# Optimization experiments

Measured on AMD Instinct MI355X. Metric: run time of the kernel, lower is better.

The kernel has to match this reference:

```python
import jax, jax.numpy as jnp
import numpy as np

D_MODEL = 1024
NUM_HEADS = 16
HEAD_DIM = D_MODEL // NUM_HEADS
ROPE_THETA = 10000.0


def apply_rope(x, positions):
    # x: (B, H, S, Dh), positions: (S,) int
    half = x.shape[-1] // 2
    inv_freq = ROPE_THETA ** (-jnp.arange(half, dtype=jnp.float32) * 2.0 / x.shape[-1])  # (Dh/2,)
    ang = positions.astype(jnp.float32)[:, None] * inv_freq[None, :]  # (S, Dh/2)
    cos, sin = jnp.cos(ang), jnp.sin(ang)
    x1 = x[..., 0::2]  # (B,H,S,Dh/2)
    x2 = x[..., 1::2]
    r1 = x1 * cos - x2 * sin
    r2 = x1 * sin + x2 * cos
    return jnp.stack([r1, r2], axis=-1).reshape(x.shape)


def setup_inputs() -> dict:
    key = jax.random.key(0)
    ks = jax.random.split(key, 5)
    B, S = 2, 2048
    scale = 1.0 / np.sqrt(D_MODEL)
    x = jax.random.normal(ks[0], (B, S, D_MODEL), dtype=jnp.float32)
    Wq = jax.random.normal(ks[1], (D_MODEL, D_MODEL), dtype=jnp.float32) * scale
    Wk = jax.random.normal(ks[2], (D_MODEL, D_MODEL), dtype=jnp.float32) * scale
    Wv = jax.random.normal(ks[3], (D_MODEL, D_MODEL), dtype=jnp.float32) * scale
    Wo = jax.random.normal(ks[4], (D_MODEL, D_MODEL), dtype=jnp.float32) * scale
    token_positions = jnp.arange(S, dtype=jnp.int32)
    return {"x": x, "token_positions": token_positions, "Wq": Wq, "Wk": Wk, "Wv": Wv, "Wo": Wo}


def reference(x, token_positions, Wq, Wk, Wv, Wo):
    B, S, _ = x.shape
    # Linear is bias-free: y = x @ W.T (W: [out, in])
    def proj(W):
        y = jnp.einsum('bsd,ed->bse', x, W)
        return y.reshape(B, S, NUM_HEADS, HEAD_DIM).transpose(0, 2, 1, 3)  # (B,H,S,Dh)
    q, k, v = proj(Wq), proj(Wk), proj(Wv)
    q = apply_rope(q, token_positions)
    k = apply_rope(k, token_positions)
    scores = jnp.einsum('bhqd,bhkd->bhqk', q, k) / jnp.sqrt(jnp.float32(HEAD_DIM))
    causal = jnp.tril(jnp.ones((S, S), dtype=bool))
    scores = jnp.where(causal, scores, -jnp.inf)
    attn = jax.nn.softmax(scores, axis=-1)
    out = jnp.einsum('bhqk,bhkd->bhqd', attn, v)  # (B,H,S,Dh)
    out = out.transpose(0, 2, 1, 3).reshape(B, S, D_MODEL)
    return jnp.einsum('bsd,ed->bse', out, Wo)
```

## Files before the change

kernel.cpp:

```cpp
#include <hip/hip_runtime.h>


typedef unsigned short u16;
typedef unsigned int   u32;
typedef unsigned long long u64;
using s16x8 = __attribute__((ext_vector_type(8))) short;
using f32x4 = __attribute__((ext_vector_type(4))) float;

__device__ __forceinline__ u16 f2bf(float f) {
  union { float f; u32 u; } v; v.f = f;
  return (u16)((v.u + 0x7fffu + ((v.u >> 16) & 1u)) >> 16);
}
__device__ __forceinline__ float bf2f(u16 h) {
  union { u32 u; float f; } v; v.u = ((u32)h) << 16;
  return v.f;
}

__device__ __forceinline__ void gl2lds(const u16* g, u16* l) {
  __builtin_amdgcn_global_load_lds(
      (const __attribute__((address_space(1))) void*)g,
      (__attribute__((address_space(3))) void*)l, 16, 0, 0);
}

__global__ __launch_bounds__(256) void cvt_all(
    const float* __restrict__ x,
    const float* __restrict__ wq, const float* __restrict__ wk,
    const float* __restrict__ wv, const float* __restrict__ wo,
    u16* __restrict__ xb, u16* __restrict__ wqb, u16* __restrict__ wkb,
    u16* __restrict__ wvb, u16* __restrict__ wob,
    float* __restrict__ rtab, const int* __restrict__ pos) {
  int bid = blockIdx.x;
  if (bid >= 8192) {
    int idx = (bid - 8192) * 256 + threadIdx.x;
    int s = idx >> 5, pair = idx & 31;
    float p = (float)pos[s];
    float freq = __expf(-0.28782313662425572f * (float)pair);
    float sn, cs;
    sincosf(p * freq, &sn, &cs);
    *(float2*)(rtab + idx * 2) = make_float2(cs, sn);
    return;
  }
  int e = (bid * 256 + threadIdx.x) * 4;
  const float* src; u16* dst; int off;
  const int XN = 4 << 20;
  if (e < XN) { src = x; dst = xb; off = e; }
  else {
    int t = e - XN; int sel = t >> 20; off = t & ((1 << 20) - 1);
    src = sel == 0 ? wq : sel == 1 ? wk : sel == 2 ? wv : wo;
    dst = sel == 0 ? wqb : sel == 1 ? wkb : sel == 2 ? wvb : wob;
  }
  float4 v = *(const float4*)(src + off);
  ushort4 o;
  o.x = f2bf(v.x); o.y = f2bf(v.y); o.z = f2bf(v.z); o.w = f2bf(v.w);
  *(ushort4*)(dst + off) = o;
}

__device__ __forceinline__ void gemm_core(
    const u16* __restrict__ A, const u16* __restrict__ W,
    u16* As, u16* Bs, int bm0, int bn0, int kb, int ke, f32x4 (&acc)[4][4]) {
  const int K = 1024;
  int tid = threadIdx.x;
  int wid = tid >> 6, lane = tid & 63, quad = lane >> 4, l15 = lane & 15;
  int wm = (wid >> 1) * 64, wn = (wid & 1) * 64;
  int ch0 = wid * 128 + lane, ch1 = ch0 + 64;
  int r0 = ch0 >> 2, c0 = (ch0 & 3) * 8;
  int r1 = ch1 >> 2, c1 = (ch1 & 3) * 8;
  const u16* Ab = A + (size_t)bm0 * K;
  const u16* Wb = W + (size_t)bn0 * K;
  u16* lA0 = As + wid * 1024; u16* lA1 = lA0 + 512;
  u16* lB0 = Bs + wid * 1024; u16* lB1 = lB0 + 512;
  for (int k0 = kb; k0 < ke; k0 += 32) {
    __syncthreads();
    gl2lds(Ab + (size_t)r0 * K + k0 + c0, lA0);
    gl2lds(Ab + (size_t)r1 * K + k0 + c1, lA1);
    gl2lds(Wb + (size_t)r0 * K + k0 + c0, lB0);
    gl2lds(Wb + (size_t)r1 * K + k0 + c1, lB1);
    __syncthreads();
    s16x8 af[4], bf[4];
#pragma unroll
    for (int mi = 0; mi < 4; mi++)
      af[mi] = *(const s16x8*)(As + (wm + mi * 16 + l15) * 32 + quad * 8);
#pragma unroll
    for (int ni = 0; ni < 4; ni++)
      bf[ni] = *(const s16x8*)(Bs + (wn + ni * 16 + l15) * 32 + quad * 8);
#pragma unroll
    for (int mi = 0; mi < 4; mi++)
#pragma unroll
      for (int ni = 0; ni < 4; ni++)
        acc[mi][ni] = __builtin_amdgcn_mfma_f32_16x16x32_bf16(
            af[mi], bf[ni], acc[mi][ni], 0, 0, 0);
  }
}

template <bool TAB>
__global__ __launch_bounds__(256) void gemm_qkv_t(
    const u16* __restrict__ xb,
    const u16* __restrict__ wq, const u16* __restrict__ wk,
    const u16* __restrict__ wv, const int* __restrict__ pos,
    const float* __restrict__ rtab,
    u16* __restrict__ qh, u16* __restrict__ kh, u16* __restrict__ vt) {
  __shared__ __align__(16) u16 As[128 * 32];
  __shared__ __align__(16) u16 Bs[128 * 32];
  __shared__ __align__(16) float tabl[TAB ? 2 : 128 * 32 * 2];
  int z = blockIdx.z;
  const u16* W = (z == 0) ? wq : (z == 1) ? wk : wv;
  int bm0 = blockIdx.y * 128, bn0 = blockIdx.x * 128;
  int tid = threadIdx.x;
  if (!TAB && z < 2) {
    for (int idx = tid; idx < 4096; idx += 256) {
      int rl = idx >> 5, pair = idx & 31;
      int s = (bm0 + rl) & 2047;
      float p = (float)pos[s];
      float freq = __expf(-0.28782313662425572f * (float)pair);
      float sn, cs;
      sincosf(p * freq, &sn, &cs);
      tabl[idx * 2] = cs;
      tabl[idx * 2 + 1] = sn;
    }
  }
  f32x4 acc[4][4];
  const f32x4 fz = {0.f, 0.f, 0.f, 0.f};
#pragma unroll
  for (int mi = 0; mi < 4; mi++)
#pragma unroll
    for (int ni = 0; ni < 4; ni++) acc[mi][ni] = fz;
  gemm_core(xb, W, As, Bs, bm0, bn0, 0, 1024, acc);
  int wid = tid >> 6, lane = tid & 63;
  int quad = lane >> 4, l15 = lane & 15;
  int wm = (wid >> 1) * 64, wn = (wid & 1) * 64;
  if (z < 2) {
    u16* dst = (z == 0) ? qh : kh;
    float qs = (z == 0) ? 0.125f : 1.0f;
#pragma unroll
    for (int mi = 0; mi < 4; mi++)
#pragma unroll
      for (int ni = 0; ni < 4; ni++) {
        int col = bn0 + wn + ni * 16 + l15;
        int h = col >> 6, d = col & 63;
        int pairi = d >> 1;
        int odd = d & 1;
#pragma unroll
        for (int r = 0; r < 4; r++) {
          int rl = wm + mi * 16 + quad * 4 + r;
          int row = bm0 + rl;
          int b = row >> 11, s = row & 2047;
          float v0 = acc[mi][ni][r];
          float vp = __shfl_xor(v0, 1, 64);
          float cs, sn;
          if (TAB) {
            float2 t = *(const float2*)(rtab + (size_t)(s * 32 + pairi) * 2);
            cs = t.x; sn = t.y;
          } else {
            cs = tabl[(rl * 32 + pairi) * 2];
            sn = tabl[(rl * 32 + pairi) * 2 + 1];
          }
          float o = odd ? (vp * sn + v0 * cs) : (v0 * cs - vp * sn);
          dst[(((size_t)(b * 16 + h)) * 2048 + s) * 64 + d] = f2bf(o * qs);
        }
      }
  } else {
#pragma unroll
    for (int mi = 0; mi < 4; mi++)
#pragma unroll
      for (int ni = 0; ni < 4; ni++) {
        int row0 = bm0 + wm + mi * 16 + quad * 4;
        int col = bn0 + wn + ni * 16 + l15;
        int b = row0 >> 11, s0 = row0 & 2047, h = col >> 6, d = col & 63;
        u64 pk = (u64)f2bf(acc[mi][ni][0]) |
                 ((u64)f2bf(acc[mi][ni][1]) << 16) |
                 ((u64)f2bf(acc[mi][ni][2]) << 32) |
                 ((u64)f2bf(acc[mi][ni][3]) << 48);
        *(u64*)(vt + (((size_t)(b * 16 + h)) * 64 + d) * 2048 + s0) = pk;
      }
  }
}

__global__ __launch_bounds__(256) void gemm_out_sk(
    const u16* __restrict__ ao, const u16* __restrict__ wo,
    float* __restrict__ pbuf) {
  __shared__ __align__(16) u16 As[128 * 32];
  __shared__ __align__(16) u16 Bs[128 * 32];
  int bm0 = blockIdx.y * 128, bn0 = blockIdx.x * 128;
  int kb = blockIdx.z * 512;
  f32x4 acc[4][4];
  const f32x4 fz = {0.f, 0.f, 0.f, 0.f};
#pragma unroll
  for (int mi = 0; mi < 4; mi++)
#pragma unroll
    for (int ni = 0; ni < 4; ni++) acc[mi][ni] = fz;
  gemm_core(ao, wo, As, Bs, bm0, bn0, kb, kb + 512, acc);
  int tid = threadIdx.x, wid = tid >> 6, lane = tid & 63;
  int quad = lane >> 4, l15 = lane & 15;
  int wm = (wid >> 1) * 64, wn = (wid & 1) * 64;
  float* dst = pbuf + (size_t)blockIdx.z * (4u << 20);
#pragma unroll
  for (int mi = 0; mi < 4; mi++)
#pragma unroll
    for (int ni = 0; ni < 4; ni++)
#pragma unroll
      for (int r = 0; r < 4; r++) {
        int row = bm0 + wm + mi * 16 + quad * 4 + r;
        int col = bn0 + wn + ni * 16 + l15;
        dst[(size_t)row * 1024 + col] = acc[mi][ni][r];
      }
}

__global__ __launch_bounds__(256) void add_out(
    const float* __restrict__ p, float* __restrict__ o) {
  int i = (blockIdx.x * 256 + threadIdx.x) * 4;
  float4 a = *(const float4*)(p + i);
  float4 b = *(const float4*)(p + (4u << 20) + i);
  float4 r;
  r.x = a.x + b.x; r.y = a.y + b.y; r.z = a.z + b.z; r.w = a.w + b.w;
  *(float4*)(o + i) = r;
}

__global__ __launch_bounds__(256) void gemm_out(
    const u16* __restrict__ ao, const u16* __restrict__ wo,
    float* __restrict__ out) {
  __shared__ __align__(16) u16 As[128 * 32];
  __shared__ __align__(16) u16 Bs[128 * 32];
  int bm0 = blockIdx.y * 128, bn0 = blockIdx.x * 128;
  f32x4 acc[4][4];
  const f32x4 fz = {0.f, 0.f, 0.f, 0.f};
#pragma unroll
  for (int mi = 0; mi < 4; mi++)
#pragma unroll
    for (int ni = 0; ni < 4; ni++) acc[mi][ni] = fz;
  gemm_core(ao, wo, As, Bs, bm0, bn0, 0, 1024, acc);
  int tid = threadIdx.x, wid = tid >> 6, lane = tid & 63;
  int quad = lane >> 4, l15 = lane & 15;
  int wm = (wid >> 1) * 64, wn = (wid & 1) * 64;
#pragma unroll
  for (int mi = 0; mi < 4; mi++)
#pragma unroll
    for (int ni = 0; ni < 4; ni++)
#pragma unroll
      for (int r = 0; r < 4; r++) {
        int row = bm0 + wm + mi * 16 + quad * 4 + r;
        int col = bn0 + wn + ni * 16 + l15;
        out[(size_t)row * 1024 + col] = acc[mi][ni][r];
      }
}

#define KTS 72
#define VTS 72
#define PTS 40
#define OTS 72

__global__ __launch_bounds__(256, 4) void attn_k(
    const u16* __restrict__ qh, const u16* __restrict__ kh,
    const u16* __restrict__ vt, u16* __restrict__ ao) {
  __shared__ __align__(16) u16 ks[64 * KTS];
  __shared__ __align__(16) u16 vs[64 * VTS];
  __shared__ __align__(16) u16 pt[4 * 16 * PTS];
  int bid = blockIdx.x;
  int bh = bid & 31, pi = bid >> 5;
  int b = bh >> 4, h = bh & 15;
  int tid = threadIdx.x, wid = tid >> 6, lane = tid & 63;
  int quad = lane >> 4, l15 = lane & 15;
  int qsub = wid & 1, thalf = wid >> 1;
  const u16* qbase = qh + (size_t)bh * 2048 * 64;
  const u16* kbase = kh + (size_t)bh * 2048 * 64;
  const u16* vbase = vt + (size_t)bh * 64 * 2048;
  u16* ptw = pt + wid * 16 * PTS;
  const f32x4 fz = {0.f, 0.f, 0.f, 0.f};
  int srow = tid >> 2, sc = (tid & 3) * 8;

#pragma unroll
  for (int phase = 0; phase < 2; phase++) {
    int qt = phase ? (63 - pi) : pi;
    int q0 = qt * 32, q0w = q0 + qsub * 16;
    s16x8 qf0 = *(const s16x8*)(qbase + (size_t)(q0w + l15) * 64 + quad * 8);
    s16x8 qf1 = *(const s16x8*)(qbase + (size_t)(q0w + l15) * 64 + 32 + quad * 8);
    f32x4 acc[4];
#pragma unroll
    for (int md = 0; md < 4; md++) acc[md] = fz;
    float lsum = 0.f;
    int qg = q0w + l15;
    int nt = (qt >> 1) + 1;
    uint4 rk0 = *(const uint4*)(kbase + (size_t)srow * 64 + sc);
    uint4 rk1 = *(const uint4*)(kbase + (size_t)srow * 64 + sc + 32);
    uint4 rv0 = *(const uint4*)(vbase + (size_t)srow * 2048 + sc);
    uint4 rv1 = *(const uint4*)(vbase + (size_t)srow * 2048 + sc + 32);
    for (int it = 0; it < nt; it++) {
      __syncthreads();
      *(uint4*)(ks + srow * KTS + sc) = rk0;
      *(uint4*)(ks + srow * KTS + sc + 32) = rk1;
      *(uint4*)(vs + srow * VTS + sc) = rv0;
      *(uint4*)(vs + srow * VTS + sc + 32) = rv1;
      if (it + 1 < nt) {
        int t1 = (it + 1) << 6;
        rk0 = *(const uint4*)(kbase + (size_t)(t1 + srow) * 64 + sc);
        rk1 = *(const uint4*)(kbase + (size_t)(t1 + srow) * 64 + sc + 32);
        rv0 = *(const uint4*)(vbase + (size_t)srow * 2048 + t1 + sc);
        rv1 = *(const uint4*)(vbase + (size_t)srow * 2048 + t1 + sc + 32);
      }
      __syncthreads();
      int t0 = it << 6, tb = thalf * 32;
      bool diag = (it == nt - 1);
#pragma unroll
      for (int mt = 0; mt < 2; mt++) {
        int krow = tb + mt * 16 + l15;
        s16x8 ka0 = *(const s16x8*)(ks + krow * KTS + quad * 8);
        s16x8 ka1 = *(const s16x8*)(ks + krow * KTS + 32 + quad * 8);
        f32x4 st = __builtin_amdgcn_mfma_f32_16x16x32_bf16(ka0, qf0, fz, 0, 0, 0);
        st = __builtin_amdgcn_mfma_f32_16x16x32_bf16(ka1, qf1, st, 0, 0, 0);
        u64 pk = 0;
#pragma unroll
        for (int r = 0; r < 4; r++) {
          float p = __expf(st[r]);
          if (diag) {
            int tg = t0 + tb + mt * 16 + quad * 4 + r;
            if (tg > qg) p = 0.f;
          }
          lsum += p;
          pk |= ((u64)f2bf(p)) << (16 * r);
        }
        *(u64*)(ptw + l15 * PTS + mt * 16 + quad * 4) = pk;
      }
      s16x8 pb = *(const s16x8*)(ptw + l15 * PTS + quad * 8);
#pragma unroll
      for (int md = 0; md < 4; md++) {
        s16x8 va = *(const s16x8*)(vs + (md * 16 + l15) * VTS + tb + quad * 8);
        acc[md] = __builtin_amdgcn_mfma_f32_16x16x32_bf16(va, pb, acc[md], 0, 0, 0);
      }
    }
    lsum += __shfl_xor(lsum, 16, 64);
    lsum += __shfl_xor(lsum, 32, 64);
    __syncthreads();
    float* redo = (float*)ks;
    float* redl = (float*)vs;
    if (thalf == 1) {
#pragma unroll
      for (int md = 0; md < 4; md++)
#pragma unroll
        for (int r = 0; r < 4; r++)
          redo[(qsub * 64 + lane) * 16 + md * 4 + r] = acc[md][r];
      redl[qsub * 64 + lane] = lsum;
    }
    __syncthreads();
    if (thalf == 0) {
#pragma unroll
      for (int md = 0; md < 4; md++)
#pragma unroll
        for (int r = 0; r < 4; r++)
          acc[md][r] += redo[(qsub * 64 + lane) * 16 + md * 4 + r];
      lsum += redl[qsub * 64 + lane];
      float rl = 1.0f / lsum;
      u16* ow = pt + qsub * 16 * OTS;
#pragma unroll
      for (int md = 0; md < 4; md++) {
        u64 ok = 0;
#pragma unroll
        for (int r = 0; r < 4; r++)
          ok |= ((u64)f2bf(acc[md][r] * rl)) << (16 * r);
        *(u64*)(ow + l15 * OTS + md * 16 + quad * 4) = ok;
      }
      int qq = lane >> 2, dc = lane & 3;
      uint4 o0 = *(uint4*)(ow + qq * OTS + dc * 16);
      uint4 o1 = *(uint4*)(ow + qq * OTS + dc * 16 + 8);
      size_t orow = (size_t)b * 2048 + q0 + qsub * 16 + qq;
      *(uint4*)(ao + orow * 1024 + h * 64 + dc * 16) = o0;
      *(uint4*)(ao + orow * 1024 + h * 64 + dc * 16 + 8) = o1;
    }
  }
}

extern "C" void kernel_launch(void* const* d_in, const int* in_sizes, int n_in,
                              void* d_out, int out_size, void* d_ws,
                              size_t ws_size, hipStream_t stream) {
  const float* x  = (const float*)d_in[0];
  const int* pos  = (const int*)d_in[1];
  const float* Wq = (const float*)d_in[2];
  const float* Wk = (const float*)d_in[3];
  const float* Wv = (const float*)d_in[4];
  const float* Wo = (const float*)d_in[5];
  float* out = (float*)d_out;

  char* ws = (char*)d_ws;
  const size_t MB = 1u << 20;
  u16* xb  = (u16*)(ws);
  u16* wqb = (u16*)(ws + 8 * MB);
  u16* wkb = (u16*)(ws + 10 * MB);
  u16* wvb = (u16*)(ws + 12 * MB);
  u16* wob = (u16*)(ws + 14 * MB);
  u16* qhb = (u16*)(ws + 16 * MB);
  u16* khb = (u16*)(ws + 24 * MB);
  u16* vtb = (u16*)(ws + 32 * MB);
  float* rtab = (float*)(ws + 40 * MB);
  float* pbuf = (float*)(ws + 41 * MB);
  u16* ao  = xb;

  bool tabok = ws_size >= 41 * MB;
  bool skok  = ws_size >= 73 * MB;

  cvt_all<<<tabok ? 8448 : 8192, 256, 0, stream>>>(
      x, Wq, Wk, Wv, Wo, xb, wqb, wkb, wvb, wob, rtab, pos);
  if (tabok)
    gemm_qkv_t<true><<<dim3(8, 32, 3), 256, 0, stream>>>(
        xb, wqb, wkb, wvb, pos, rtab, qhb, khb, vtb);
  else
    gemm_qkv_t<false><<<dim3(8, 32, 3), 256, 0, stream>>>(
        xb, wqb, wkb, wvb, pos, rtab, qhb, khb, vtb);
  attn_k<<<1024, 256, 0, stream>>>(qhb, khb, vtb, ao);
  if (skok) {
    gemm_out_sk<<<dim3(8, 32, 2), 256, 0, stream>>>(ao, wob, pbuf);
    add_out<<<4096, 256, 0, stream>>>(pbuf, out);
  } else {
    gemm_out<<<dim3(8, 32), 256, 0, stream>>>(ao, wob, out);
  }
}
```

Measured before the change: 207.5 us.

## Remap GEMM block order, stage QK epilogue through LDS, widen attention blocks

The QKV and output GEMMs now remap the linear block index so consecutive blocks are spread across tiles, aiming for better cache and XCD locality. The Q/K RoPE epilogue writes to a padded LDS tile first and then issues coalesced 16-byte stores, replacing scattered 2-byte global writes. The attention kernel moves to 512-thread blocks covering 64 query rows, so each K/V tile loaded into LDS is shared by twice as many queries. That halves the grid to 512 blocks and adds LDS use, which may reduce occupancy and makes the diagonal tile larger.

```diff
diff --git a/kernel.cpp b/kernel.cpp
--- a/kernel.cpp
+++ b/kernel.cpp
@@ -101,10 +101,13 @@
     u16* __restrict__ qh, u16* __restrict__ kh, u16* __restrict__ vt) {
   __shared__ __align__(16) u16 As[128 * 32];
   __shared__ __align__(16) u16 Bs[128 * 32];
+  __shared__ __align__(16) u16 ob[128 * 136];
   __shared__ __align__(16) float tabl[TAB ? 2 : 128 * 32 * 2];
-  int z = blockIdx.z;
+  int id = blockIdx.x + 8 * blockIdx.y + 256 * blockIdx.z;
+  int nid = (id & 7) * 96 + (id >> 3);
+  int bx = nid & 7, by = (nid >> 3) & 31, z = nid >> 8;
   const u16* W = (z == 0) ? wq : (z == 1) ? wk : wv;
-  int bm0 = blockIdx.y * 128, bn0 = blockIdx.x * 128;
+  int bm0 = by * 128, bn0 = bx * 128;
   int tid = threadIdx.x;
   if (!TAB && z < 2) {
     for (int idx = tid; idx < 4096; idx += 256) {
@@ -135,15 +138,13 @@
     for (int mi = 0; mi < 4; mi++)
 #pragma unroll
       for (int ni = 0; ni < 4; ni++) {
-        int col = bn0 + wn + ni * 16 + l15;
-        int h = col >> 6, d = col & 63;
-        int pairi = d >> 1;
-        int odd = d & 1;
+        int col = wn + ni * 16 + l15;
+        int d = (bn0 + col) & 63;
+        int pairi = d >> 1, odd = d & 1;
 #pragma unroll
         for (int r = 0; r < 4; r++) {
           int rl = wm + mi * 16 + quad * 4 + r;
-          int row = bm0 + rl;
-          int b = row >> 11, s = row & 2047;
+          int s = (bm0 + rl) & 2047;
           float v0 = acc[mi][ni][r];
           float vp = __shfl_xor(v0, 1, 64);
           float cs, sn;
@@ -155,9 +156,21 @@
             sn = tabl[(rl * 32 + pairi) * 2 + 1];
           }
           float o = odd ? (vp * sn + v0 * cs) : (v0 * cs - vp * sn);
-          dst[(((size_t)(b * 16 + h)) * 2048 + s) * 64 + d] = f2bf(o * qs);
+          ob[rl * 136 + col] = f2bf(o * qs);
         }
       }
+    __syncthreads();
+#pragma unroll
+    for (int k2 = 0; k2 < 8; k2++) {
+      int idx = tid + 256 * k2;
+      int row = idx >> 4, seg = idx & 15;
+      uint4 w = *(const uint4*)(ob + row * 136 + seg * 8);
+      int grow = bm0 + row;
+      int b2 = grow >> 11, s2 = grow & 2047;
+      int gc = bn0 + seg * 8;
+      int h2 = gc >> 6, d2 = gc & 63;
+      *(uint4*)(dst + (((size_t)(b2 * 16 + h2)) * 2048 + s2) * 64 + d2) = w;
+    }
   } else {
 #pragma unroll
     for (int mi = 0; mi < 4; mi++)
@@ -180,8 +193,11 @@
     float* __restrict__ pbuf) {
   __shared__ __align__(16) u16 As[128 * 32];
   __shared__ __align__(16) u16 Bs[128 * 32];
-  int bm0 = blockIdx.y * 128, bn0 = blockIdx.x * 128;
-  int kb = blockIdx.z * 512;
+  int id = blockIdx.x + 8 * blockIdx.y + 256 * blockIdx.z;
+  int nid = (id & 7) * 64 + (id >> 3);
+  int bx = nid & 7, by = (nid >> 3) & 31, z = nid >> 8;
+  int bm0 = by * 128, bn0 = bx * 128;
+  int kb = z * 512;
   f32x4 acc[4][4];
   const f32x4 fz = {0.f, 0.f, 0.f, 0.f};
 #pragma unroll
@@ -192,7 +208,7 @@
   int tid = threadIdx.x, wid = tid >> 6, lane = tid & 63;
   int quad = lane >> 4, l15 = lane & 15;
   int wm = (wid >> 1) * 64, wn = (wid & 1) * 64;
-  float* dst = pbuf + (size_t)blockIdx.z * (4u << 20);
+  float* dst = pbuf + (size_t)z * (4u << 20);
 #pragma unroll
   for (int mi = 0; mi < 4; mi++)
 #pragma unroll
@@ -248,29 +264,32 @@
 #define PTS 40
 #define OTS 72
 
-__global__ __launch_bounds__(256, 4) void attn_k(
+__global__ __launch_bounds__(512, 4) void attn_k(
     const u16* __restrict__ qh, const u16* __restrict__ kh,
     const u16* __restrict__ vt, u16* __restrict__ ao) {
-  __shared__ __align__(16) u16 ks[64 * KTS];
-  __shared__ __align__(16) u16 vs[64 * VTS];
-  __shared__ __align__(16) u16 pt[4 * 16 * PTS];
+  __shared__ __align__(16) u16 kv[64 * KTS + 64 * VTS];
+  __shared__ __align__(16) u16 pt[8 * 16 * PTS];
+  __shared__ __align__(16) float redl2[256];
+  u16* ks = kv;
+  u16* vs = kv + 64 * KTS;
   int bid = blockIdx.x;
   int bh = bid & 31, pi = bid >> 5;
   int b = bh >> 4, h = bh & 15;
   int tid = threadIdx.x, wid = tid >> 6, lane = tid & 63;
   int quad = lane >> 4, l15 = lane & 15;
-  int qsub = wid & 1, thalf = wid >> 1;
+  int qsub = wid & 3, thalf = wid >> 2;
   const u16* qbase = qh + (size_t)bh * 2048 * 64;
   const u16* kbase = kh + (size_t)bh * 2048 * 64;
   const u16* vbase = vt + (size_t)bh * 64 * 2048;
   u16* ptw = pt + wid * 16 * PTS;
   const f32x4 fz = {0.f, 0.f, 0.f, 0.f};
-  int srow = tid >> 2, sc = (tid & 3) * 8;
+  int srow = tid >> 3, sc = (tid & 7) * 8;
+  int tb = thalf * 32;
 
 #pragma unroll
   for (int phase = 0; phase < 2; phase++) {
-    int qt = phase ? (63 - pi) : pi;
-    int q0 = qt * 32, q0w = q0 + qsub * 16;
+    int qt = phase ? (31 - pi) : pi;
+    int q0 = qt * 64, q0w = q0 + qsub * 16;
     s16x8 qf0 = *(const s16x8*)(qbase + (size_t)(q0w + l15) * 64 + quad * 8);
     s16x8 qf1 = *(const s16x8*)(qbase + (size_t)(q0w + l15) * 64 + 32 + quad * 8);
     f32x4 acc[4];
@@ -278,26 +297,20 @@
     for (int md = 0; md < 4; md++) acc[md] = fz;
     float lsum = 0.f;
     int qg = q0w + l15;
-    int nt = (qt >> 1) + 1;
+    int nt = qt + 1;
     uint4 rk0 = *(const uint4*)(kbase + (size_t)srow * 64 + sc);
-    uint4 rk1 = *(const uint4*)(kbase + (size_t)srow * 64 + sc + 32);
     uint4 rv0 = *(const uint4*)(vbase + (size_t)srow * 2048 + sc);
-    uint4 rv1 = *(const uint4*)(vbase + (size_t)srow * 2048 + sc + 32);
     for (int it = 0; it < nt; it++) {
       __syncthreads();
       *(uint4*)(ks + srow * KTS + sc) = rk0;
-      *(uint4*)(ks + srow * KTS + sc + 32) = rk1;
       *(uint4*)(vs + srow * VTS + sc) = rv0;
-      *(uint4*)(vs + srow * VTS + sc + 32) = rv1;
       if (it + 1 < nt) {
         int t1 = (it + 1) << 6;
         rk0 = *(const uint4*)(kbase + (size_t)(t1 + srow) * 64 + sc);
-        rk1 = *(const uint4*)(kbase + (size_t)(t1 + srow) * 64 + sc + 32);
         rv0 = *(const uint4*)(vbase + (size_t)srow * 2048 + t1 + sc);
-        rv1 = *(const uint4*)(vbase + (size_t)srow * 2048 + t1 + sc + 32);
       }
       __syncthreads();
-      int t0 = it << 6, tb = thalf * 32;
+      int t0 = it << 6;
       bool diag = (it == nt - 1);
 #pragma unroll
       for (int mt = 0; mt < 2; mt++) {
@@ -329,15 +342,14 @@
     lsum += __shfl_xor(lsum, 16, 64);
     lsum += __shfl_xor(lsum, 32, 64);
     __syncthreads();
-    float* redo = (float*)ks;
-    float* redl = (float*)vs;
+    float* redo = (float*)kv;
     if (thalf == 1) {
 #pragma unroll
       for (int md = 0; md < 4; md++)
 #pragma unroll
         for (int r = 0; r < 4; r++)
           redo[(qsub * 64 + lane) * 16 + md * 4 + r] = acc[md][r];
-      redl[qsub * 64 + lane] = lsum;
+      redl2[qsub * 64 + lane] = lsum;
     }
     __syncthreads();
     if (thalf == 0) {
@@ -346,7 +358,7 @@
 #pragma unroll
         for (int r = 0; r < 4; r++)
           acc[md][r] += redo[(qsub * 64 + lane) * 16 + md * 4 + r];
-      lsum += redl[qsub * 64 + lane];
+      lsum += redl2[qsub * 64 + lane];
       float rl = 1.0f / lsum;
       u16* ow = pt + qsub * 16 * OTS;
 #pragma unroll
@@ -403,7 +415,7 @@
   else
     gemm_qkv_t<false><<<dim3(8, 32, 3), 256, 0, stream>>>(
         xb, wqb, wkb, wvb, pos, rtab, qhb, khb, vtb);
-  attn_k<<<1024, 256, 0, stream>>>(qhb, khb, vtb, ao);
+  attn_k<<<512, 512, 0, stream>>>(qhb, khb, vtb, ao);
   if (skok) {
     gemm_out_sk<<<dim3(8, 32, 2), 256, 0, stream>>>(ao, wob, pbuf);
     add_out<<<4096, 256, 0, stream>>>(pbuf, out);
```

After: 196.0 us. 1.06x faster.
